# Kernel optimization log

Hardware: AMD Instinct MI355X
Metric: run time of the kernel (lower is better)

The kernel has to match this reference:

```python
import jax, jax.numpy as jnp
import numpy as np


def setup_inputs() -> dict:
    key = jax.random.key(0)
    B, L, d_model, d_state, expand = 2, 2048, 1024, 16, 2
    d_inner = expand * d_model
    ks = jax.random.split(key, 8)
    s = lambda k, shape, scale: jax.random.normal(k, shape, dtype=jnp.float32) * scale
    x = s(ks[0], (B, L, d_model), 1.0)
    W_in = s(ks[1], (d_model, 2 * d_inner), 0.02)     # in_proj (no bias)
    W_delta = s(ks[2], (d_inner, d_inner), 0.02)      # delta_proj weight
    b_delta = s(ks[3], (d_inner,), 0.02)              # delta_proj bias
    W_B = s(ks[4], (d_inner, d_state), 0.02)          # B_proj (no bias)
    W_C = s(ks[5], (d_inner, d_state), 0.02)          # C_proj (no bias)
    # A_log = log(repeat(arange(1, d_state+1), 'n -> d n'))
    A_log = jnp.log(jnp.broadcast_to(
        jnp.arange(1, d_state + 1, dtype=jnp.float32), (d_inner, d_state)))
    D_param = jnp.ones((d_inner,), dtype=jnp.float32)
    W_out = s(ks[6], (d_inner, d_model), 0.02)        # out_proj (no bias)
    return dict(x=x, W_in=W_in, W_delta=W_delta, b_delta=b_delta,
                W_B=W_B, W_C=W_C, A_log=A_log, D_param=D_param, W_out=W_out)


def reference(x, W_in, W_delta, b_delta, W_B, W_C, A_log, D_param, W_out):
    d_inner = W_delta.shape[0]
    # in_proj then split into ssm branch (u) and gate (res)
    x_and_res = x @ W_in                       # (B, L, 2*d_inner)
    u, res = x_and_res[..., :d_inner], x_and_res[..., d_inner:]
    u = jax.nn.silu(u)                         # (B, L, d_inner)

    # input-dependent SSM parameters
    delta = jax.nn.softplus(u @ W_delta + b_delta)   # (B, L, d_inner)
    Bm = u @ W_B                                     # (B, L, d_state)
    Cm = u @ W_C                                     # (B, L, d_state)
    A = -jnp.exp(A_log)                              # (d_inner, d_state)

    def step(h, inp):
        d_t, B_t, C_t, u_t = inp  # (B,d), (B,n), (B,n), (B,d)
        dA = jnp.exp(d_t[..., None] * A)                          # (B,d,n)
        h = dA * h + d_t[..., None] * B_t[:, None, :] * u_t[..., None]
        y_t = jnp.einsum('bdn,bn->bd', h, C_t)
        return h, y_t

    Bsz = x.shape[0]
    h0 = jnp.zeros((Bsz, d_inner, A.shape[1]), dtype=x.dtype)
    xs = (jnp.swapaxes(delta, 0, 1), jnp.swapaxes(Bm, 0, 1),
          jnp.swapaxes(Cm, 0, 1), jnp.swapaxes(u, 0, 1))
    _, ys = jax.lax.scan(step, h0, xs)          # ys: (L, B, d_inner)
    y = jnp.swapaxes(ys, 0, 1) + u * D_param    # skip connection with D

    y = y * jax.nn.silu(res)                    # gating
    return y @ W_out                            # (B, L, d_model)
```

## Files before the change

kernel.cpp:

```cpp
#include <hip/hip_runtime.h>
#include <hip/hip_bf16.h>

typedef unsigned short ushort_t;
typedef __bf16 bf16x8 __attribute__((ext_vector_type(8)));
typedef float f32x4 __attribute__((ext_vector_type(4)));

typedef const void __attribute__((address_space(1)))* gas1_t;
typedef void __attribute__((address_space(3)))* las3_t;

#define L_SZ 2048
#define DI   2048
#define M_ROWS 4096
#define NC 64
#define TC 32

__device__ __forceinline__ float bf2f(ushort_t u){
  unsigned x = ((unsigned)u) << 16; float f; __builtin_memcpy(&f, &x, 4); return f;
}
__device__ __forceinline__ ushort_t f2bf(float f){
  __hip_bfloat16 h = __float2bfloat16(f);
  ushort_t u; __builtin_memcpy(&u, &h, 2); return u;
}
__device__ __forceinline__ float siluf(float x){ return x / (1.0f + __expf(-x)); }
__device__ __forceinline__ float softplusf(float x){
  return (x > 20.0f) ? x : log1pf(__expf(x));
}

__global__ __launch_bounds__(256) void k_prep(
    const float* __restrict__ W_in, const float* __restrict__ W_delta,
    const float* __restrict__ W_out, const float* __restrict__ W_B,
    const float* __restrict__ W_C, const float* __restrict__ x,
    ushort_t* __restrict__ W_inT, ushort_t* __restrict__ W_bigT,
    ushort_t* __restrict__ W_outT, ushort_t* __restrict__ xb)
{
  int t = blockIdx.x;
  if (t >= 10368){
    size_t i = (size_t)(t - 10368) * 256 + threadIdx.x;
    float4 v = *(const float4*)(x + i * 4);
    ushort_t o[4] = { f2bf(v.x), f2bf(v.y), f2bf(v.z), f2bf(v.w) };
    *(uint2*)(xb + i * 4) = *(const uint2*)o;
    return;
  }
  const float* in; ushort_t* out; int R, C, tx, ty;
  if (t < 4096)      { in=W_in;    out=W_inT;  R=1024; C=4096; tx = t & 127; ty = t >> 7; }
  else if (t < 8192) { t -= 4096;  in=W_delta; out=W_bigT; R=2048; C=2048; tx = t & 63; ty = t >> 6; }
  else if (t < 10240){ t -= 8192;  in=W_out;   out=W_outT; R=2048; C=1024; tx = t & 31; ty = t >> 5; }
  else if (t < 10304){ t -= 10240; in=W_B;  out=W_bigT + (size_t)2048*2048; R=2048; C=16; tx=0; ty=t; }
  else               { t -= 10304; in=W_C;  out=W_bigT + (size_t)2064*2048; R=2048; C=16; tx=0; ty=t; }
  __shared__ ushort_t tile[32][33];
  int c0 = tx * 32, r0 = ty * 32;
  int xx = threadIdx.x & 31, yy = threadIdx.x >> 5;
  #pragma unroll
  for (int i = 0; i < 32; i += 8){
    int r = r0 + yy + i, c = c0 + xx;
    if (r < R && c < C) tile[yy + i][xx] = f2bf(in[(size_t)r * C + c]);
  }
  __syncthreads();
  #pragma unroll
  for (int i = 0; i < 32; i += 8){
    int c = c0 + yy + i, r = r0 + xx;
    if (r < R && c < C) out[(size_t)c * R + r] = tile[xx][yy + i];
  }
}

template<int BM, int BN, int EPI>
__global__ __launch_bounds__(256) void k_gemm_bt(
    const ushort_t* __restrict__ A, int lda,
    const ushort_t* __restrict__ Bt, int ldb,
    void* __restrict__ Cout, int ldc,
    const float* __restrict__ bias,
    float* __restrict__ Bm, float* __restrict__ Cm, int K)
{
  constexpr int WM = BM/2, WN = BN/2;
  constexpr int MT = WM/16, NT = WN/16;
  constexpr int ACH = BM*16;
  constexpr int BCH = BN*16;
  constexpr int NISSUE = (ACH+BCH)/256;
  __shared__ __align__(16) char lds[(BM+BN)*256];
  char* ldsA = lds;
  char* ldsB = lds + BM*256;
  const int tid  = threadIdx.x;
  const int wave = tid >> 6, lane = tid & 63;
  const int quad = lane >> 4, l16 = lane & 15;
  const int m_blk = blockIdx.y * BM, n_blk = blockIdx.x * BN;
  const int wm = (wave >> 1) * WM, wn = (wave & 1) * WN;

  f32x4 acc[MT][NT] = {};

  const ushort_t* gptr[NISSUE];
  char* lptr[NISSUE];
  #pragma unroll
  for (int i = 0; i < NISSUE; i++){
    int g = tid + i*256;
    if (g < ACH){
      int sl = (g >= ACH/2) ? 1 : 0;
      int gl = g - sl*(ACH/2);
      int row = gl >> 3, c = gl & 7;
      gptr[i] = A + (size_t)(m_blk + row) * lda + sl*64 + ((c ^ (row & 7)) * 8);
    } else {
      int gb = g - ACH;
      int sl = (gb >= BCH/2) ? 1 : 0;
      int gl = gb - sl*(BCH/2);
      int row = gl >> 3, c = gl & 7;
      gptr[i] = Bt + (size_t)(n_blk + row) * ldb + sl*64 + ((c ^ (row & 7)) * 8);
    }
    lptr[i] = lds + (size_t)g*16;
  }

  const int xsw = (l16 & 7);

  for (int k0 = 0; k0 < K; k0 += 128){
    #pragma unroll
    for (int i = 0; i < NISSUE; i++)
      __builtin_amdgcn_global_load_lds((gas1_t)(const void*)(gptr[i] + k0), (las3_t)lptr[i], 16, 0, 0);
    __syncthreads();
    #pragma unroll
    for (int sl = 0; sl < 2; sl++){
      #pragma unroll
      for (int s = 0; s < 2; s++){
        const int xa = ((s*4 + quad) ^ xsw) * 16;
        bf16x8 af[MT], bfr[NT];
        #pragma unroll
        for (int i = 0; i < MT; i++)
          af[i]  = *(const bf16x8*)(ldsA + sl*(BM*128) + (wm + i * 16 + l16) * 128 + xa);
        #pragma unroll
        for (int i = 0; i < NT; i++)
          bfr[i] = *(const bf16x8*)(ldsB + sl*(BN*128) + (wn + i * 16 + l16) * 128 + xa);
        #pragma unroll
        for (int mt = 0; mt < MT; mt++)
          #pragma unroll
          for (int nt = 0; nt < NT; nt++)
            acc[mt][nt] = __builtin_amdgcn_mfma_f32_16x16x32_bf16(af[mt], bfr[nt], acc[mt][nt], 0, 0, 0);
      }
    }
    __syncthreads();
  }

  #pragma unroll
  for (int mt = 0; mt < MT; mt++){
    #pragma unroll
    for (int nt = 0; nt < NT; nt++){
      #pragma unroll
      for (int r = 0; r < 4; r++){
        int m = m_blk + wm + mt * 16 + quad * 4 + r;
        int n = n_blk + wn + nt * 16 + l16;
        float v = acc[mt][nt][r];
        if (EPI == 0){
          ((float*)Cout)[(size_t)m * ldc + n] = v;
        } else if (EPI == 1){
          ((__hip_bfloat16*)Cout)[(size_t)m * ldc + n] = __float2bfloat16(siluf(v));
        } else {
          if (n < 2048)      ((ushort_t*)Cout)[(size_t)m * ldc + n] = f2bf(softplusf(v + bias[n]));
          else if (n < 2064) Bm[(size_t)m * 16 + (n - 2048)] = v;
          else if (n < 2080) Cm[(size_t)m * 16 + (n - 2064)] = v;
        }
      }
    }
  }
}

__device__ __forceinline__ void load_An(const float* A_log, int d, float* An){
  const float* ap = A_log + (size_t)d * 16;
  #pragma unroll
  for (int j = 0; j < 16; j += 4){
    float4 v = *(const float4*)(ap + j);
    An[j]   = -__expf(v.x);
    An[j+1] = -__expf(v.y);
    An[j+2] = -__expf(v.z);
    An[j+3] = -__expf(v.w);
  }
}

__global__ __launch_bounds__(256) void k_scan1(
    const ushort_t* __restrict__ delta, const ushort_t* __restrict__ U,
    const float* __restrict__ Bm, const float* __restrict__ A_log,
    float* __restrict__ q, float* __restrict__ S)
{
  __shared__ float ldsB[TC * 16];
  const int tid = threadIdx.x;
  const int ch  = blockIdx.x * 256 + tid;
  const int b   = ch >> 11, d = ch & 2047;
  const int c   = blockIdx.y;
  const int t0  = c * TC;
  if (tid < 128){
    int tt = tid >> 2, n4 = (tid & 3) * 4;
    *(float4*)&ldsB[tt * 16 + n4] = *(const float4*)&Bm[((size_t)b * L_SZ + t0 + tt) * 16 + n4];
  }
  float An[16];
  load_An(A_log, d, An);
  __syncthreads();
  float h[16];
  #pragma unroll
  for (int j = 0; j < 16; j++) h[j] = 0.f;
  float Ssum = 0.f;
  const size_t row0 = (size_t)b * L_SZ + t0;
  for (int ti = 0; ti < TC; ti += 4){
    float dlt[4], uv[4];
    #pragma unroll
    for (int k = 0; k < 4; k++){
      size_t row = row0 + ti + k;
      dlt[k] = bf2f(delta[row * DI + d]);
      uv[k]  = bf2f(U[row * 4096 + d]);
    }
    #pragma unroll
    for (int k = 0; k < 4; k++){
      float du = dlt[k] * uv[k];
      Ssum += dlt[k];
      #pragma unroll
      for (int nn = 0; nn < 16; nn++)
        h[nn] = fmaf(__expf(dlt[k] * An[nn]), h[nn], du * ldsB[(ti + k) * 16 + nn]);
    }
  }
  size_t qb = ((size_t)c * M_ROWS + ch) * 16;
  #pragma unroll
  for (int j = 0; j < 16; j += 4)
    *(float4*)&q[qb + j] = make_float4(h[j], h[j+1], h[j+2], h[j+3]);
  S[(size_t)c * M_ROWS + ch] = Ssum;
}

__global__ __launch_bounds__(256) void k_scan_combine(
    const float* __restrict__ q, const float* __restrict__ S,
    const float* __restrict__ A_log, float* __restrict__ hin)
{
  int gid = blockIdx.x * 256 + threadIdx.x;
  int ch = gid >> 4, nn = gid & 15, d = ch & 2047;
  float An = -__expf(A_log[(size_t)d * 16 + nn]);
  float h = 0.f;
  for (int c = 0; c < NC; c++){
    size_t base = (size_t)c * M_ROWS + ch;
    hin[base * 16 + nn] = h;
    h = fmaf(__expf(An * S[base]), h, q[base * 16 + nn]);
  }
}

__global__ __launch_bounds__(256) void k_scan2(
    const ushort_t* __restrict__ delta, const ushort_t* __restrict__ U,
    const float* __restrict__ Bm, const float* __restrict__ Cm,
    const float* __restrict__ A_log, const float* __restrict__ Dpar,
    const float* __restrict__ hin, ushort_t* __restrict__ Y)
{
  __shared__ float ldsBC[TC * 16 * 2];
  const int tid = threadIdx.x;
  const int ch  = blockIdx.x * 256 + tid;
  const int b   = ch >> 11, d = ch & 2047;
  const int c   = blockIdx.y;
  const int t0  = c * TC;
  {
    int tt = tid >> 3, n2 = (tid & 7) * 2;
    size_t gb = ((size_t)b * L_SZ + t0 + tt) * 16 + n2;
    float2 bv = *(const float2*)&Bm[gb];
    float2 cv = *(const float2*)&Cm[gb];
    float2* dst = (float2*)&ldsBC[(tt * 16 + n2) * 2];
    dst[0] = make_float2(bv.x, cv.x);
    dst[1] = make_float2(bv.y, cv.y);
  }
  float An[16];
  load_An(A_log, d, An);
  float Dv = Dpar[d];
  __syncthreads();
  float h[16];
  size_t hb = ((size_t)c * M_ROWS + ch) * 16;
  #pragma unroll
  for (int j = 0; j < 16; j += 4){
    float4 hv = *(const float4*)&hin[hb + j];
    h[j] = hv.x; h[j+1] = hv.y; h[j+2] = hv.z; h[j+3] = hv.w;
  }
  const size_t row0 = (size_t)b * L_SZ + t0;
  for (int ti = 0; ti < TC; ti += 4){
    float dlt[4], uv[4], sres[4];
    #pragma unroll
    for (int k = 0; k < 4; k++){
      size_t row = row0 + ti + k;
      dlt[k]  = bf2f(delta[row * DI + d]);
      uv[k]   = bf2f(U[row * 4096 + d]);
      sres[k] = bf2f(U[row * 4096 + 2048 + d]);
    }
    ushort_t yo[4];
    #pragma unroll
    for (int k = 0; k < 4; k++){
      float du = dlt[k] * uv[k];
      float y = 0.f;
      #pragma unroll
      for (int nn = 0; nn < 16; nn++){
        float2 bc = *(const float2*)&ldsBC[((ti + k) * 16 + nn) * 2];
        h[nn] = fmaf(__expf(dlt[k] * An[nn]), h[nn], du * bc.x);
        y = fmaf(h[nn], bc.y, y);
      }
      yo[k] = f2bf((y + uv[k] * Dv) * sres[k]);
    }
    #pragma unroll
    for (int k = 0; k < 4; k++)
      Y[(row0 + ti + k) * DI + d] = yo[k];
  }
}

extern "C" void kernel_launch(void* const* d_in, const int* in_sizes, int n_in,
                              void* d_out, int out_size, void* d_ws, size_t ws_size,
                              hipStream_t stream)
{
  const float* x       = (const float*)d_in[0];
  const float* W_in    = (const float*)d_in[1];
  const float* W_delta = (const float*)d_in[2];
  const float* b_delta = (const float*)d_in[3];
  const float* W_B     = (const float*)d_in[4];
  const float* W_C     = (const float*)d_in[5];
  const float* A_log   = (const float*)d_in[6];
  const float* D_par   = (const float*)d_in[7];
  const float* W_out   = (const float*)d_in[8];

  char* ws = (char*)d_ws;
  size_t off = 0;
  auto alloc = [&](size_t bytes){ char* p = ws + off; off += (bytes + 255) & ~(size_t)255; return p; };
  ushort_t* W_inT  = (ushort_t*)alloc((size_t)4096*1024*2);
  ushort_t* W_bigT = (ushort_t*)alloc((size_t)2176*2048*2);
  ushort_t* W_outT = (ushort_t*)alloc((size_t)1024*2048*2);
  ushort_t* xb     = (ushort_t*)alloc((size_t)4096*1024*2);
  ushort_t* U      = (ushort_t*)alloc((size_t)4096*4096*2);
  ushort_t* dl     = (ushort_t*)alloc((size_t)4096*2048*2);
  float*    Bm     = (float*)alloc((size_t)4096*16*4);
  float*    Cm     = (float*)alloc((size_t)4096*16*4);
  float*    qbuf   = (float*)alloc((size_t)NC*4096*16*4);
  float*    Sbuf   = (float*)alloc((size_t)NC*4096*4);
  float*    hin    = (float*)alloc((size_t)NC*4096*16*4);
  ushort_t* Y      = (ushort_t*)alloc((size_t)4096*2048*2);

  k_prep<<<dim3(14464),256,0,stream>>>(W_in, W_delta, W_out, W_B, W_C, x,
                                       W_inT, W_bigT, W_outT, xb);

  k_gemm_bt<128,64,1><<<dim3(64,32),256,0,stream>>>(xb, 1024, W_inT, 1024, U, 4096,
                                                    nullptr, nullptr, nullptr, 1024);

  k_gemm_bt<128,64,2><<<dim3(33,32),256,0,stream>>>(U, 4096, W_bigT, 2048, dl, 2048,
                                                    b_delta, Bm, Cm, 2048);

  k_scan1<<<dim3(16,NC),256,0,stream>>>(dl, U, Bm, A_log, qbuf, Sbuf);
  k_scan_combine<<<dim3(256),256,0,stream>>>(qbuf, Sbuf, A_log, hin);
  k_scan2<<<dim3(16,NC),256,0,stream>>>(dl, U, Bm, Cm, A_log, D_par, hin, Y);

  k_gemm_bt<64,64,0><<<dim3(16,64),256,0,stream>>>(Y, 2048, W_outT, 2048, d_out, 1024,
                                                   nullptr, nullptr, nullptr, 2048);
}
```

Measured before the change: 352.7 us.

## Add 256x256 pipelined GEMM with direct-to-LDS loads for input and delta projections

Adds a new 512-thread GEMM kernel for the in_proj and delta/B/C projection GEMMs, replacing the 128x64-tile kernel. It uses 256x256 block tiles, double-buffered 64-wide K slices, and global_load_lds staging interleaved across four compute phases per buffer, with XOR-swizzled LDS layout and MFMA priority boosting. The aim is more data reuse per tile and better overlap of memory loads with MFMA work. The trade-off is 128KB LDS per block, so only one block fits per CU. The delta GEMM also launches just 144 blocks, which may leave CUs idle. The fused weight buffer is padded to 2304 rows to fit the tile size.

```diff
diff --git a/kernel.cpp b/kernel.cpp
--- a/kernel.cpp
+++ b/kernel.cpp
@@ -159,6 +159,122 @@
   }
 }
 
+
+#define STG_A(d,H,T) { \
+  __builtin_amdgcn_global_load_lds((gas1_t)(const void*)(gA + (size_t)(H)*128*lda + (size_t)(T)*64), \
+      (las3_t)(void*)(lds + (d)*65536 + (H)*16384 + tid*16), 16, 0, 0); \
+  __builtin_amdgcn_global_load_lds((gas1_t)(const void*)(gA + ((size_t)(H)*128+64)*lda + (size_t)(T)*64), \
+      (las3_t)(void*)(lds + (d)*65536 + (H)*16384 + 8192 + tid*16), 16, 0, 0); }
+
+#define STG_B(d,H,T) { \
+  __builtin_amdgcn_global_load_lds((gas1_t)(const void*)(gB + (size_t)(H)*128*ldb + (size_t)(T)*64), \
+      (las3_t)(void*)(lds + (d)*65536 + 32768 + (H)*16384 + tid*16), 16, 0, 0); \
+  __builtin_amdgcn_global_load_lds((gas1_t)(const void*)(gB + ((size_t)(H)*128+64)*ldb + (size_t)(T)*64), \
+      (las3_t)(void*)(lds + (d)*65536 + 32768 + (H)*16384 + 8192 + tid*16), 16, 0, 0); }
+
+#define PHASE(d, qm, qn, ...) { \
+  bf16x8 af0[4], af1[4], bq0[2], bq1[2]; \
+  const char* pA_ = lds + (d)*65536 + ((qm)*128 + wm*64 + l16)*128; \
+  const char* pB_ = lds + (d)*65536 + 32768 + ((qn)*128 + wn*32 + l16)*128; \
+  const int x0_ = ((0*4 + quad) ^ xsw) * 16; \
+  const int x1_ = ((1*4 + quad) ^ xsw) * 16; \
+  _Pragma("unroll") \
+  for (int mt = 0; mt < 4; mt++){ \
+    af0[mt] = *(const bf16x8*)(pA_ + mt*2048 + x0_); \
+    af1[mt] = *(const bf16x8*)(pA_ + mt*2048 + x1_); } \
+  _Pragma("unroll") \
+  for (int nt = 0; nt < 2; nt++){ \
+    bq0[nt] = *(const bf16x8*)(pB_ + nt*2048 + x0_); \
+    bq1[nt] = *(const bf16x8*)(pB_ + nt*2048 + x1_); } \
+  __VA_ARGS__ \
+  __builtin_amdgcn_s_barrier(); \
+  asm volatile("s_waitcnt lgkmcnt(0)" ::: "memory"); \
+  __builtin_amdgcn_sched_barrier(0); \
+  __builtin_amdgcn_s_setprio(1); \
+  _Pragma("unroll") \
+  for (int mt = 0; mt < 4; mt++){ \
+    _Pragma("unroll") \
+    for (int nt = 0; nt < 2; nt++){ \
+      acc[qm][qn][mt][nt] = __builtin_amdgcn_mfma_f32_16x16x32_bf16(af0[mt], bq0[nt], acc[qm][qn][mt][nt], 0, 0, 0); \
+      acc[qm][qn][mt][nt] = __builtin_amdgcn_mfma_f32_16x16x32_bf16(af1[mt], bq1[nt], acc[qm][qn][mt][nt], 0, 0, 0); } } \
+  __builtin_amdgcn_s_setprio(0); }
+
+#define TBAR __builtin_amdgcn_s_barrier()
+
+template<int EPI>
+__global__ __launch_bounds__(512, 2) void k_gemm256(
+    const ushort_t* __restrict__ A, int lda,
+    const ushort_t* __restrict__ Bt, int ldb,
+    void* __restrict__ Cout, int ldc,
+    const float* __restrict__ bias,
+    float* __restrict__ Bm, float* __restrict__ Cm, int K)
+{
+  __shared__ __align__(16) char lds[131072];
+  const int tid  = threadIdx.x;
+  const int wave = tid >> 6, lane = tid & 63;
+  const int quad = lane >> 4, l16 = lane & 15;
+  const int wm = wave >> 2;
+  const int wn = wave & 3;
+  const int m_blk = blockIdx.y * 256, n_blk = blockIdx.x * 256;
+  const int xsw = l16 & 7;
+
+  const int srow = tid >> 3;
+  const int schk = tid & 7;
+  const ushort_t* gA = A  + (size_t)(m_blk + srow) * lda + ((schk ^ (srow & 7)) * 8);
+  const ushort_t* gB = Bt + (size_t)(n_blk + srow) * ldb + ((schk ^ (srow & 7)) * 8);
+
+  f32x4 acc[2][2][4][2] = {};
+
+  const int NTK = K >> 6;
+
+  STG_A(0,0,0); STG_B(0,0,0); STG_A(0,1,0); STG_B(0,1,0);
+  STG_B(1,0,1); STG_A(1,0,1);
+  asm volatile("s_waitcnt vmcnt(4)" ::: "memory");
+  __builtin_amdgcn_s_barrier();
+
+  for (int T = 0; T < NTK; T += 2){
+    PHASE(0,0,0, STG_A(1,1,T+1);) TBAR;
+    PHASE(0,1,0, STG_B(1,1,T+1);) TBAR;
+    PHASE(0,0,1, if (T+2 < NTK) STG_B(0,0,T+2);) TBAR;
+    PHASE(0,1,1, if (T+2 < NTK) STG_A(0,0,T+2);)
+    if (T+2 < NTK) { asm volatile("s_waitcnt vmcnt(4)" ::: "memory"); }
+    else           { asm volatile("s_waitcnt vmcnt(0)" ::: "memory"); }
+    TBAR;
+    PHASE(1,0,0, if (T+2 < NTK) STG_A(0,1,T+2);) TBAR;
+    PHASE(1,1,0, if (T+2 < NTK) STG_B(0,1,T+2);) TBAR;
+    PHASE(1,0,1, if (T+3 < NTK) STG_B(1,0,T+3);) TBAR;
+    PHASE(1,1,1, if (T+3 < NTK) STG_A(1,0,T+3);)
+    asm volatile("s_waitcnt vmcnt(4)" ::: "memory");
+    TBAR;
+  }
+
+  #pragma unroll
+  for (int qm = 0; qm < 2; qm++){
+    #pragma unroll
+    for (int qn = 0; qn < 2; qn++){
+      #pragma unroll
+      for (int mt = 0; mt < 4; mt++){
+        #pragma unroll
+        for (int nt = 0; nt < 2; nt++){
+          #pragma unroll
+          for (int r = 0; r < 4; r++){
+            int m = m_blk + qm*128 + wm*64 + mt*16 + quad*4 + r;
+            int n = n_blk + qn*128 + wn*32 + nt*16 + l16;
+            float v = acc[qm][qn][mt][nt][r];
+            if (EPI == 1){
+              ((__hip_bfloat16*)Cout)[(size_t)m * ldc + n] = __float2bfloat16(siluf(v));
+            } else {
+              if (n < 2048)      ((ushort_t*)Cout)[(size_t)m * ldc + n] = f2bf(softplusf(v + bias[n]));
+              else if (n < 2064) Bm[(size_t)m * 16 + (n - 2048)] = v;
+              else if (n < 2080) Cm[(size_t)m * 16 + (n - 2064)] = v;
+            }
+          }
+        }
+      }
+    }
+  }
+}
+
 __device__ __forceinline__ void load_An(const float* A_log, int d, float* An){
   const float* ap = A_log + (size_t)d * 16;
   #pragma unroll
@@ -312,7 +428,7 @@
   size_t off = 0;
   auto alloc = [&](size_t bytes){ char* p = ws + off; off += (bytes + 255) & ~(size_t)255; return p; };
   ushort_t* W_inT  = (ushort_t*)alloc((size_t)4096*1024*2);
-  ushort_t* W_bigT = (ushort_t*)alloc((size_t)2176*2048*2);
+  ushort_t* W_bigT = (ushort_t*)alloc((size_t)2304*2048*2);
   ushort_t* W_outT = (ushort_t*)alloc((size_t)1024*2048*2);
   ushort_t* xb     = (ushort_t*)alloc((size_t)4096*1024*2);
   ushort_t* U      = (ushort_t*)alloc((size_t)4096*4096*2);
@@ -327,11 +443,11 @@
   k_prep<<<dim3(14464),256,0,stream>>>(W_in, W_delta, W_out, W_B, W_C, x,
                                        W_inT, W_bigT, W_outT, xb);
 
-  k_gemm_bt<128,64,1><<<dim3(64,32),256,0,stream>>>(xb, 1024, W_inT, 1024, U, 4096,
-                                                    nullptr, nullptr, nullptr, 1024);
-
-  k_gemm_bt<128,64,2><<<dim3(33,32),256,0,stream>>>(U, 4096, W_bigT, 2048, dl, 2048,
-                                                    b_delta, Bm, Cm, 2048);
+  k_gemm256<1><<<dim3(16,16),512,0,stream>>>(xb, 1024, W_inT, 1024, U, 4096,
+                                             nullptr, nullptr, nullptr, 1024);
+
+  k_gemm256<2><<<dim3(9,16),512,0,stream>>>(U, 4096, W_bigT, 2048, dl, 2048,
+                                            b_delta, Bm, Cm, 2048);
 
   k_scan1<<<dim3(16,NC),256,0,stream>>>(dl, U, Bm, A_log, qbuf, Sbuf);
   k_scan_combine<<<dim3(256),256,0,stream>>>(qbuf, Sbuf, A_log, hin);
```

New measurement: 392.9 us. 1.11x slower.
